# Kernel tuning notes

Hardware: AMD Instinct MI355X
Metric: run time of the kernel (lower is better)

The kernel has to match this reference:

```python
import jax, jax.numpy as jnp
import numpy as np

B, T, D = 2, 2048, 2048
N_HEADS, N_KV, HEAD_DIM = 16, 8, 128
SOFTCAP = 50.0
BIG_NEG = -2.3819763e38
ROPE_BASE = 10000.0


def apply_rope(x, positions):
    # x: [B, L, N, H], positions: [B, L]
    H = x.shape[-1]
    half = H // 2
    fraction = 2.0 * jnp.arange(half, dtype=jnp.float32) / H
    timescale = ROPE_BASE ** fraction  # [H/2]
    sinusoid = positions.astype(jnp.float32)[:, :, None, None] / timescale[None, None, None, :]  # [B,L,1,H/2]
    sin, cos = jnp.sin(sinusoid), jnp.cos(sinusoid)
    first, second = jnp.split(x, 2, axis=-1)
    out = jnp.concatenate([first * cos - second * sin, second * cos + first * sin], axis=-1)
    return out.astype(x.dtype)


def setup_inputs() -> dict:
    key = jax.random.key(0)
    k1, k2, k3, k4 = jax.random.split(key, 4)
    x = jax.random.normal(k1, (B, T, D), dtype=jnp.float32)
    positions = jnp.broadcast_to(jnp.arange(T, dtype=jnp.int32), (B, T))
    # causal mask [B, 1, T, S]
    attn_mask = jnp.broadcast_to(jnp.tril(jnp.ones((T, T), dtype=bool))[None, None], (B, 1, T, T))
    s = 1.0 / np.sqrt(D)
    w_q = jax.random.normal(k2, (N_HEADS, D, HEAD_DIM), dtype=jnp.float32) * s
    w_kv = jax.random.normal(k3, (2, N_KV, D, HEAD_DIM), dtype=jnp.float32) * s
    w_out = jax.random.normal(k4, (N_HEADS, HEAD_DIM, D), dtype=jnp.float32) * (1.0 / np.sqrt(N_HEADS * HEAD_DIM))
    return {"x": x, "positions": positions, "attn_mask": attn_mask, "w_q": w_q, "w_kv": w_kv, "w_out": w_out}


def reference(x, positions, attn_mask, w_q, w_kv, w_out):
    # projections (GQA branch: num_kv_heads != num_heads)
    q = jnp.einsum('btd,ndh->btnh', x, w_q)            # [B,T,N,H]
    kv = jnp.einsum('bsd,cndh->cbsnh', x, w_kv)        # [2,B,S,K,H]
    k, v = kv[0], kv[1]
    q = apply_rope(q, positions) * (HEAD_DIM ** -0.5)  # rsqrt_head_dim
    k = apply_rope(k, positions)
    G = N_HEADS // N_KV
    q = q.reshape(B, T, N_KV, G, HEAD_DIM)             # B T K G H
    logits = jnp.einsum('btkgh,bskh->bkgts', q, k).astype(jnp.float32)
    logits = jnp.tanh(logits / SOFTCAP) * SOFTCAP
    masked = jnp.where(attn_mask[:, :, None, :, :], logits, BIG_NEG)
    probs = jax.nn.softmax(masked, axis=-1).astype(k.dtype)
    encoded = jnp.einsum('bkgts,bskh->btkgh', probs, v).reshape(B, T, N_HEADS, HEAD_DIM)
    return jnp.einsum('btnh,nhd->btd', encoded, w_out)
```

## Files before the change

### kernel.cpp

```cpp
#include <hip/hip_runtime.h>


typedef unsigned short u16;
typedef __attribute__((ext_vector_type(8))) short short8;
typedef __attribute__((ext_vector_type(4))) float floatx4;

static __device__ __forceinline__ u16 f2b(float f){
  unsigned u = __float_as_uint(f);
  u = (u + 0x7fffu + ((u >> 16) & 1u)) >> 16;
  return (u16)u;
}
static __device__ __forceinline__ float b2f(u16 u){
  return __uint_as_float(((unsigned)u) << 16);
}
static __device__ __forceinline__ void gload16(const u16* g, u16* l){
  __builtin_amdgcn_global_load_lds(
      (const __attribute__((address_space(1))) unsigned int*)g,
      (__attribute__((address_space(3))) unsigned int*)l, 16, 0, 0);
}

static __device__ void tr64(const float* __restrict__ s, u16* __restrict__ d,
                            int sRS, int dRS, float (*t)[65], int tid){
  #pragma unroll
  for(int i = 0; i < 16; i++){
    int idx = tid + 256 * i;
    t[idx >> 6][idx & 63] = s[(long)(idx >> 6) * sRS + (idx & 63)];
  }
  __syncthreads();
  #pragma unroll
  for(int i = 0; i < 16; i++){
    int idx = tid + 256 * i;
    d[(long)(idx >> 6) * dRS + (idx & 63)] = f2b(t[idx & 63][idx >> 6]);
  }
}

__global__ __launch_bounds__(256) void k_prep(
    const float* __restrict__ x, u16* __restrict__ xb,
    const float* __restrict__ wq, u16* __restrict__ wq_t,
    const float* __restrict__ wkv, u16* __restrict__ wkv_t,
    const float* __restrict__ wo, u16* __restrict__ wo_t,
    const int* __restrict__ pos, float* __restrict__ tab){
  __shared__ float t[64][65];
  int blk = blockIdx.x, tid = threadIdx.x;
  if(blk < 8192){
    int i = blk * 256 + tid;
    float4 v = ((const float4*)x)[i];
    ushort4 o = make_ushort4(f2b(v.x), f2b(v.y), f2b(v.z), f2b(v.w));
    ((ushort4*)xb)[i] = o;
  } else if(blk < 9216){
    int q = blk - 8192;
    int bx = q & 1, by = (q >> 1) & 31, bz = q >> 6;
    tr64(wq + (long)bz * 262144 + (long)by * 64 * 128 + bx * 64,
         wq_t + (long)bz * 262144 + (long)bx * 64 * 2048 + by * 64, 128, 2048, t, tid);
  } else if(blk < 10240){
    int q = blk - 9216;
    int bx = q & 1, by = (q >> 1) & 31, bz = q >> 6;
    tr64(wkv + (long)bz * 262144 + (long)by * 64 * 128 + bx * 64,
         wkv_t + (long)bz * 262144 + (long)bx * 64 * 2048 + by * 64, 128, 2048, t, tid);
  } else if(blk < 11264){
    int q = blk - 10240;
    int bx = q & 31, by = q >> 5;
    tr64(wo + (long)by * 64 * 2048 + bx * 64,
         wo_t + (long)bx * 64 * 2048 + by * 64, 2048, 2048, t, tid);
  } else {
    int idx = (blk - 11264) * 256 + tid;
    int row = idx >> 6, h = idx & 63;
    float pf = (float)pos[row];
    float inv = exp2f(-0.20762050593045077f * (float)h);
    float ang = pf * inv;
    tab[(row << 7) + h]      = sinf(ang);
    tab[(row << 7) + 64 + h] = cosf(ang);
  }
}

__global__ __launch_bounds__(256) void k_gemm_qkv(
    const u16* __restrict__ A, const u16* __restrict__ wq_t, const u16* __restrict__ wkv_t,
    const float* __restrict__ tab,
    u16* __restrict__ qb, u16* __restrict__ kb, u16* __restrict__ vtp){
  __shared__ __attribute__((aligned(16))) u16 pool[128 * 132];
  u16* sA = pool;
  u16* sB = pool + 8192;
  int mt = blockIdx.x, nt = blockIdx.y;
  const u16* Bt = (nt < 16) ? (wq_t + (long)nt * 262144)
                            : (wkv_t + (long)(nt - 16) * 262144);
  int tid = threadIdx.x;
  int lane = tid & 63, wave = tid >> 6, l15 = lane & 15, quad = lane >> 4;
  int ro = (wave & 1) * 64, co = (wave >> 1) * 64;
  int xm7 = l15 & 7;
  int srow = tid >> 3;
  int gch  = (tid & 7) ^ (srow & 7);
  const u16* Ag = A  + ((long)(mt * 128) + srow) * 2048 + (gch << 3);
  const u16* Bg = Bt + (long)srow * 2048 + (gch << 3);
  u16* lA = sA + tid * 8;
  u16* lB = sB + tid * 8;
  floatx4 acc[4][4];
  const floatx4 fz = {0.f, 0.f, 0.f, 0.f};
  #pragma unroll
  for(int r = 0; r < 4; r++)
    #pragma unroll
    for(int c = 0; c < 4; c++) acc[r][c] = fz;
  for(int k0 = 0; k0 < 2048; k0 += 64){
    #pragma unroll
    for(int r = 0; r < 4; r++){
      gload16(Ag + (long)r * 65536 + k0, lA + r * 2048);
      gload16(Bg + (long)r * 65536 + k0, lB + r * 2048);
    }
    __syncthreads();
    #pragma unroll
    for(int ks = 0; ks < 2; ks++){
      short8 af[4], bfr[4];
      #pragma unroll
      for(int r = 0; r < 4; r++)
        af[r]  = *(const short8*)(sA + ((ro + r * 16 + l15) << 6) + ((((ks << 2) | quad) ^ xm7) << 3));
      #pragma unroll
      for(int c = 0; c < 4; c++)
        bfr[c] = *(const short8*)(sB + ((co + c * 16 + l15) << 6) + ((((ks << 2) | quad) ^ xm7) << 3));
      #pragma unroll
      for(int r = 0; r < 4; r++)
        #pragma unroll
        for(int c = 0; c < 4; c++)
          acc[r][c] = __builtin_amdgcn_mfma_f32_16x16x32_bf16(af[r], bfr[c], acc[r][c], 0, 0, 0);
    }
    __syncthreads();
  }
  u16* sT = pool;
  #pragma unroll
  for(int r = 0; r < 4; r++)
    #pragma unroll
    for(int c = 0; c < 4; c++){
      int row = ro + r * 16 + quad * 4, col = co + c * 16 + l15;
      #pragma unroll
      for(int j = 0; j < 4; j++) sT[(row + j) * 132 + col] = f2b(acc[r][c][j]);
    }
  __syncthreads();
  int grow0 = mt * 128;
  if(nt < 24){
    float scale = (nt < 16) ? 0.08838834764831845f : 1.0f;
    u16* dst = (nt < 16) ? qb : kb;
    int dS   = (nt < 16) ? 2048 : 1024;
    int dcol = (nt < 16) ? nt * 128 : (nt - 16) * 128;
    #pragma unroll
    for(int it = 0; it < 16; it++){
      int idx = tid + 256 * it;
      int row = idx >> 5, cw = idx & 31;
      int grow = grow0 + row;
      unsigned lo = *(const unsigned*)&sT[row * 132 + 2 * cw];
      unsigned hi = *(const unsigned*)&sT[row * 132 + 64 + 2 * cw];
      float2 sn = *(const float2*)&tab[(grow << 7) + 2 * cw];
      float2 cs = *(const float2*)&tab[(grow << 7) + 64 + 2 * cw];
      float x1a = b2f((u16)lo), x1b = b2f((u16)(lo >> 16));
      float x2a = b2f((u16)hi), x2b = b2f((u16)(hi >> 16));
      float o1a = (x1a * cs.x - x2a * sn.x) * scale;
      float o1b = (x1b * cs.y - x2b * sn.y) * scale;
      float o2a = (x2a * cs.x + x1a * sn.x) * scale;
      float o2b = (x2b * cs.y + x1b * sn.y) * scale;
      unsigned w1 = (unsigned)f2b(o1a) | ((unsigned)f2b(o1b) << 16);
      unsigned w2 = (unsigned)f2b(o2a) | ((unsigned)f2b(o2b) << 16);
      *(unsigned*)&dst[(long)grow * dS + dcol + 2 * cw] = w1;
      *(unsigned*)&dst[(long)grow * dS + dcol + 64 + 2 * cw] = w2;
    }
  } else {
    int b = mt >> 4, kvh = nt - 24;
    u16* vt = vtp + (long)(b * 8 + kvh) * 262144;
    int tcol0 = (mt & 15) * 128;
    int h = tid >> 1, s0 = (tid & 1) * 64;
    #pragma unroll
    for(int i = 0; i < 16; i++){
      int s = s0 + i * 4;
      ushort4 v4 = make_ushort4(sT[(s    ) * 132 + h], sT[(s + 1) * 132 + h],
                                sT[(s + 2) * 132 + h], sT[(s + 3) * 132 + h]);
      *(ushort4*)&vt[(long)h * 2048 + tcol0 + s] = v4;
    }
  }
}

__global__ __launch_bounds__(256) void k_gemm_out(
    const u16* __restrict__ A, const u16* __restrict__ Bt0, float* __restrict__ C){
  __shared__ __attribute__((aligned(16))) u16 sA[128 * 64];
  __shared__ __attribute__((aligned(16))) u16 sB[128 * 64];
  int mt = blockIdx.x, nt = blockIdx.y;
  const u16* Bt = Bt0 + (long)nt * 262144;
  int tid = threadIdx.x;
  int lane = tid & 63, wave = tid >> 6, l15 = lane & 15, quad = lane >> 4;
  int ro = (wave & 1) * 64, co = (wave >> 1) * 64;
  int xm7 = l15 & 7;
  int srow = tid >> 3;
  int gch  = (tid & 7) ^ (srow & 7);
  const u16* Ag = A  + ((long)(mt * 128) + srow) * 2048 + (gch << 3);
  const u16* Bg = Bt + (long)srow * 2048 + (gch << 3);
  u16* lA = sA + tid * 8;
  u16* lB = sB + tid * 8;
  floatx4 acc[4][4];
  const floatx4 fz = {0.f, 0.f, 0.f, 0.f};
  #pragma unroll
  for(int r = 0; r < 4; r++)
    #pragma unroll
    for(int c = 0; c < 4; c++) acc[r][c] = fz;
  for(int k0 = 0; k0 < 2048; k0 += 64){
    #pragma unroll
    for(int r = 0; r < 4; r++){
      gload16(Ag + (long)r * 65536 + k0, lA + r * 2048);
      gload16(Bg + (long)r * 65536 + k0, lB + r * 2048);
    }
    __syncthreads();
    #pragma unroll
    for(int ks = 0; ks < 2; ks++){
      short8 af[4], bfr[4];
      #pragma unroll
      for(int r = 0; r < 4; r++)
        af[r]  = *(const short8*)(sA + ((ro + r * 16 + l15) << 6) + ((((ks << 2) | quad) ^ xm7) << 3));
      #pragma unroll
      for(int c = 0; c < 4; c++)
        bfr[c] = *(const short8*)(sB + ((co + c * 16 + l15) << 6) + ((((ks << 2) | quad) ^ xm7) << 3));
      #pragma unroll
      for(int r = 0; r < 4; r++)
        #pragma unroll
        for(int c = 0; c < 4; c++)
          acc[r][c] = __builtin_amdgcn_mfma_f32_16x16x32_bf16(af[r], bfr[c], acc[r][c], 0, 0, 0);
    }
    __syncthreads();
  }
  long rb0 = (long)mt * 128 + ro + quad * 4;
  #pragma unroll
  for(int r = 0; r < 4; r++)
    #pragma unroll
    for(int c = 0; c < 4; c++){
      int col = nt * 128 + co + c * 16 + l15;
      #pragma unroll
      for(int j = 0; j < 4; j++)
        C[(rb0 + r * 16 + j) * 2048 + col] = acc[r][c][j];
    }
}

__global__ __launch_bounds__(256) void k_flash(
    const u16* __restrict__ qb, const u16* __restrict__ kb,
    const u16* __restrict__ vt, u16* __restrict__ enc){
  __shared__ __attribute__((aligned(16))) u16 sK[2 * 64 * 128];
  __shared__ __attribute__((aligned(16))) u16 sVt[2 * 128 * 64];
  __shared__ __attribute__((aligned(16))) u16 sP[4][16][72];
  int qt = 31 - blockIdx.y;
  int hidx = blockIdx.x;
  int b = hidx >> 4, kv = (hidx >> 1) & 7, g = hidx & 1;
  int tid = threadIdx.x;
  int lane = tid & 63, wave = tid >> 6, l15 = lane & 15, quad = lane >> 4;

  short8 qf[4];
  {
    const u16* qg = qb + ((long)b * 2048 + qt * 64 + wave * 16 + l15) * 2048
                       + (kv * 2 + g) * 128 + quad * 8;
    #pragma unroll
    for(int ks = 0; ks < 4; ks++) qf[ks] = *(const short8*)(qg + ks * 32);
  }

  int krow = tid >> 4;
  int kch  = (tid & 15) ^ krow;
  const u16* Kg = kb + ((long)b * 2048 + krow) * 1024 + kv * 128 + (kch << 3);
  int vrow = tid >> 3;
  int vch  = (tid & 7) ^ (vrow & 7);
  const u16* Vg = vt + ((long)(b * 8 + kv) * 128 + vrow) * 2048 + (vch << 3);
  u16* lK = sK  + tid * 8;
  u16* lV = sVt + tid * 8;
  #pragma unroll
  for(int r = 0; r < 4; r++){
    gload16(Kg + (long)r * 16384, lK + r * 2048);
    gload16(Vg + (long)r * 65536, lV + r * 2048);
  }

  float l_loc[4] = {0.f, 0.f, 0.f, 0.f};
  floatx4 o_acc[8];
  const floatx4 fz = {0.f, 0.f, 0.f, 0.f};
  #pragma unroll
  for(int c = 0; c < 8; c++) o_acc[c] = fz;

  const float c1 = 0.057707801635558536f;
  const float c2 = -144.26950408889634f;
  const float c3 = 72.13475204444817f;

  for(int kt = 0; kt <= qt; kt++){
    int buf = (kt & 1) * 8192;
    __syncthreads();
    if(kt < qt){
      int nb = buf ^ 8192;
      #pragma unroll
      for(int r = 0; r < 4; r++){
        gload16(Kg + (long)(kt + 1) * 65536 + (long)r * 16384, lK + nb + r * 2048);
        gload16(Vg + (kt + 1) * 64 + (long)r * 65536, lV + nb + r * 2048);
      }
    }
    floatx4 s_acc[4];
    #pragma unroll
    for(int c = 0; c < 4; c++) s_acc[c] = fz;
    #pragma unroll
    for(int ks = 0; ks < 4; ks++){
      #pragma unroll
      for(int cb = 0; cb < 4; cb++){
        short8 bk = *(const short8*)(sK + buf + ((cb * 16 + l15) << 7)
                                     + ((((ks << 2) | quad) ^ l15) << 3));
        s_acc[cb] = __builtin_amdgcn_mfma_f32_16x16x32_bf16(qf[ks], bk, s_acc[cb], 0, 0, 0);
      }
    }
    if(kt < qt){
      #pragma unroll
      for(int r = 0; r < 4; r++){
        #pragma unroll
        for(int cb = 0; cb < 4; cb++){
          float s = s_acc[cb][r];
          float u = __builtin_amdgcn_exp2f(c1 * s);
          float d = __builtin_amdgcn_rcpf(u + 1.f);
          float p = __builtin_amdgcn_exp2f(__builtin_fmaf(c2, d, c3));
          l_loc[r] += p;
          sP[wave][quad * 4 + r][cb * 16 + l15] = f2b(p);
        }
      }
    } else {
      int rloc = wave * 16 + quad * 4;
      #pragma unroll
      for(int r = 0; r < 4; r++){
        #pragma unroll
        for(int cb = 0; cb < 4; cb++){
          float s = s_acc[cb][r];
          float u = __builtin_amdgcn_exp2f(c1 * s);
          float d = __builtin_amdgcn_rcpf(u + 1.f);
          float p = __builtin_amdgcn_exp2f(__builtin_fmaf(c2, d, c3));
          if(cb * 16 + l15 > rloc + r) p = 0.f;
          l_loc[r] += p;
          sP[wave][quad * 4 + r][cb * 16 + l15] = f2b(p);
        }
      }
    }
    #pragma unroll
    for(int ks2 = 0; ks2 < 2; ks2++){
      short8 ap = *(const short8*)&sP[wave][l15][ks2 * 32 + quad * 8];
      #pragma unroll
      for(int c = 0; c < 8; c++){
        short8 bv = *(const short8*)(sVt + buf + ((c * 16 + l15) << 6)
                                     + ((((ks2 << 2) | quad) ^ (l15 & 7)) << 3));
        o_acc[c] = __builtin_amdgcn_mfma_f32_16x16x32_bf16(ap, bv, o_acc[c], 0, 0, 0);
      }
    }
  }
  #pragma unroll
  for(int r = 0; r < 4; r++){
    float l = l_loc[r];
    #pragma unroll
    for(int off = 1; off < 16; off <<= 1) l += __shfl_xor(l, off);
    float invl = 1.f / l;
    long rowe = (long)b * 2048 + qt * 64 + wave * 16 + quad * 4 + r;
    #pragma unroll
    for(int c = 0; c < 8; c++)
      enc[rowe * 2048 + (kv * 2 + g) * 128 + c * 16 + l15] = f2b(o_acc[c][r] * invl);
  }
}

extern "C" void kernel_launch(void* const* d_in, const int* in_sizes, int n_in,
                              void* d_out, int out_size, void* d_ws, size_t ws_size,
                              hipStream_t stream){
  const float* x     = (const float*)d_in[0];
  const int*   posi  = (const int*)  d_in[1];
  const float* w_q   = (const float*)d_in[3];
  const float* w_kv  = (const float*)d_in[4];
  const float* w_out = (const float*)d_in[5];
  float* out = (float*)d_out;

  char* w = (char*)d_ws;
  u16* xb     = (u16*)(w);
  u16* wq_t   = (u16*)(w + 16777216);
  u16* wkv_t  = (u16*)(w + 25165824);
  u16* wout_t = (u16*)(w + 33554432);
  u16* q_buf  = (u16*)(w + 41943040);
  u16* k_buf  = (u16*)(w + 58720256);
  u16* v_t    = (u16*)(w + 67108864);
  float* tab  = (float*)(w + 75497472);
  u16* enc    = xb;

  k_prep    <<<12288, 256, 0, stream>>>(x, xb, w_q, wq_t, w_kv, wkv_t, w_out, wout_t, posi, tab);
  k_gemm_qkv<<<dim3(32, 32), 256, 0, stream>>>(xb, wq_t, wkv_t, tab, q_buf, k_buf, v_t);
  k_flash   <<<dim3(32, 32), 256, 0, stream>>>(q_buf, k_buf, v_t, enc);
  k_gemm_out<<<dim3(32, 16), 256, 0, stream>>>(enc, wout_t, out);
}
```

Baseline: 333.0 us.

## Split flash-attention waves 2x2 over query rows and key columns with reduction

Each wave in the attention kernel now owns 32 query rows and half of each 64-key tile, instead of 16 rows and the full tile. Each K fragment loaded from shared memory therefore feeds two MFMAs, which cuts LDS reads per MFMA for QK^T. The two key-halves accumulate partial outputs and row sums that are combined through shared memory at the end. The P buffer is reshaped with an XOR swizzle to reduce bank conflicts. In exchange the kernel holds twice the accumulator registers, which may lower occupancy, and adds a final cross-wave reduction with extra syncs.

```diff
diff --git a/kernel.cpp b/kernel.cpp
--- a/kernel.cpp
+++ b/kernel.cpp
@@ -237,19 +237,23 @@
     const u16* __restrict__ vt, u16* __restrict__ enc){
   __shared__ __attribute__((aligned(16))) u16 sK[2 * 64 * 128];
   __shared__ __attribute__((aligned(16))) u16 sVt[2 * 128 * 64];
-  __shared__ __attribute__((aligned(16))) u16 sP[4][16][72];
+  __shared__ __attribute__((aligned(16))) u16 sP[4][32][40];
   int qt = 31 - blockIdx.y;
   int hidx = blockIdx.x;
   int b = hidx >> 4, kv = (hidx >> 1) & 7, g = hidx & 1;
   int tid = threadIdx.x;
   int lane = tid & 63, wave = tid >> 6, l15 = lane & 15, quad = lane >> 4;
-
-  short8 qf[4];
+  int rq = wave >> 1, kq = wave & 1;
+
+  short8 qf[2][4];
   {
-    const u16* qg = qb + ((long)b * 2048 + qt * 64 + wave * 16 + l15) * 2048
+    const u16* qg = qb + ((long)b * 2048 + qt * 64 + rq * 32 + l15) * 2048
                        + (kv * 2 + g) * 128 + quad * 8;
     #pragma unroll
-    for(int ks = 0; ks < 4; ks++) qf[ks] = *(const short8*)(qg + ks * 32);
+    for(int rf = 0; rf < 2; rf++)
+      #pragma unroll
+      for(int ks = 0; ks < 4; ks++)
+        qf[rf][ks] = *(const short8*)(qg + rf * 16 * 2048 + ks * 32);
   }
 
   int krow = tid >> 4;
@@ -266,11 +270,13 @@
     gload16(Vg + (long)r * 65536, lV + r * 2048);
   }
 
-  float l_loc[4] = {0.f, 0.f, 0.f, 0.f};
-  floatx4 o_acc[8];
+  float l_loc[2][4] = {{0.f,0.f,0.f,0.f},{0.f,0.f,0.f,0.f}};
+  floatx4 o_acc[2][8];
   const floatx4 fz = {0.f, 0.f, 0.f, 0.f};
   #pragma unroll
-  for(int c = 0; c < 8; c++) o_acc[c] = fz;
+  for(int rf = 0; rf < 2; rf++)
+    #pragma unroll
+    for(int c = 0; c < 8; c++) o_acc[rf][c] = fz;
 
   const float c1 = 0.057707801635558536f;
   const float c2 = -144.26950408889634f;
@@ -287,68 +293,89 @@
         gload16(Vg + (kt + 1) * 64 + (long)r * 65536, lV + nb + r * 2048);
       }
     }
-    floatx4 s_acc[4];
-    #pragma unroll
-    for(int c = 0; c < 4; c++) s_acc[c] = fz;
+    floatx4 s_acc[2][2];
+    #pragma unroll
+    for(int rf = 0; rf < 2; rf++)
+      #pragma unroll
+      for(int cf = 0; cf < 2; cf++) s_acc[rf][cf] = fz;
     #pragma unroll
     for(int ks = 0; ks < 4; ks++){
       #pragma unroll
-      for(int cb = 0; cb < 4; cb++){
-        short8 bk = *(const short8*)(sK + buf + ((cb * 16 + l15) << 7)
+      for(int cf = 0; cf < 2; cf++){
+        int row = kq * 32 + cf * 16 + l15;
+        short8 bk = *(const short8*)(sK + buf + (row << 7)
                                      + ((((ks << 2) | quad) ^ l15) << 3));
-        s_acc[cb] = __builtin_amdgcn_mfma_f32_16x16x32_bf16(qf[ks], bk, s_acc[cb], 0, 0, 0);
+        #pragma unroll
+        for(int rf = 0; rf < 2; rf++)
+          s_acc[rf][cf] = __builtin_amdgcn_mfma_f32_16x16x32_bf16(qf[rf][ks], bk, s_acc[rf][cf], 0, 0, 0);
       }
     }
-    if(kt < qt){
-      #pragma unroll
-      for(int r = 0; r < 4; r++){
-        #pragma unroll
-        for(int cb = 0; cb < 4; cb++){
-          float s = s_acc[cb][r];
+    bool diag = (kt == qt);
+    #pragma unroll
+    for(int rf = 0; rf < 2; rf++)
+      #pragma unroll
+      for(int cf = 0; cf < 2; cf++)
+        #pragma unroll
+        for(int r = 0; r < 4; r++){
+          float s = s_acc[rf][cf][r];
           float u = __builtin_amdgcn_exp2f(c1 * s);
           float d = __builtin_amdgcn_rcpf(u + 1.f);
           float p = __builtin_amdgcn_exp2f(__builtin_fmaf(c2, d, c3));
-          l_loc[r] += p;
-          sP[wave][quad * 4 + r][cb * 16 + l15] = f2b(p);
+          if(diag && (kq * 32 + cf * 16 + l15 > rq * 32 + rf * 16 + quad * 4 + r)) p = 0.f;
+          l_loc[rf][r] += p;
+          int chunk = ((cf << 1) | (l15 >> 3)) ^ r;
+          sP[wave][rf * 16 + quad * 4 + r][(chunk << 3) + (l15 & 7)] = f2b(p);
         }
+    #pragma unroll
+    for(int rf = 0; rf < 2; rf++){
+      short8 ap = *(const short8*)&sP[wave][rf * 16 + l15][(quad ^ (l15 & 3)) << 3];
+      #pragma unroll
+      for(int cf = 0; cf < 8; cf++){
+        int vrw = cf * 16 + l15;
+        short8 bv = *(const short8*)(sVt + buf + (vrw << 6)
+                                     + ((((kq << 2) | quad) ^ (l15 & 7)) << 3));
+        o_acc[rf][cf] = __builtin_amdgcn_mfma_f32_16x16x32_bf16(ap, bv, o_acc[rf][cf], 0, 0, 0);
       }
-    } else {
-      int rloc = wave * 16 + quad * 4;
+    }
+  }
+  __syncthreads();
+  float* ex  = (float*)sK;
+  float* exl = (float*)sVt;
+  if(kq == 0){
+    #pragma unroll
+    for(int rf = 0; rf < 2; rf++)
+      #pragma unroll
+      for(int cf = 0; cf < 8; cf++)
+        *(floatx4*)&ex[rq * 4096 + (rf * 8 + cf) * 256 + lane * 4] = o_acc[rf][cf];
+    #pragma unroll
+    for(int rf = 0; rf < 2; rf++)
+      #pragma unroll
+      for(int r = 0; r < 4; r++)
+        exl[rq * 512 + (rf * 4 + r) * 64 + lane] = l_loc[rf][r];
+  }
+  __syncthreads();
+  if(kq == 1){
+    #pragma unroll
+    for(int rf = 0; rf < 2; rf++)
+      #pragma unroll
+      for(int cf = 0; cf < 8; cf++){
+        floatx4 o0 = *(const floatx4*)&ex[rq * 4096 + (rf * 8 + cf) * 256 + lane * 4];
+        o_acc[rf][cf] += o0;
+      }
+    #pragma unroll
+    for(int rf = 0; rf < 2; rf++){
       #pragma unroll
       for(int r = 0; r < 4; r++){
-        #pragma unroll
-        for(int cb = 0; cb < 4; cb++){
-          float s = s_acc[cb][r];
-          float u = __builtin_amdgcn_exp2f(c1 * s);
-          float d = __builtin_amdgcn_rcpf(u + 1.f);
-          float p = __builtin_amdgcn_exp2f(__builtin_fmaf(c2, d, c3));
-          if(cb * 16 + l15 > rloc + r) p = 0.f;
-          l_loc[r] += p;
-          sP[wave][quad * 4 + r][cb * 16 + l15] = f2b(p);
-        }
+        float l = l_loc[rf][r] + exl[rq * 512 + (rf * 4 + r) * 64 + lane];
+        #pragma unroll
+        for(int off = 1; off < 16; off <<= 1) l += __shfl_xor(l, off);
+        float invl = 1.f / l;
+        long rowe = (long)b * 2048 + qt * 64 + rq * 32 + rf * 16 + quad * 4 + r;
+        #pragma unroll
+        for(int cf = 0; cf < 8; cf++)
+          enc[rowe * 2048 + (kv * 2 + g) * 128 + cf * 16 + l15] = f2b(o_acc[rf][cf][r] * invl);
       }
     }
-    #pragma unroll
-    for(int ks2 = 0; ks2 < 2; ks2++){
-      short8 ap = *(const short8*)&sP[wave][l15][ks2 * 32 + quad * 8];
-      #pragma unroll
-      for(int c = 0; c < 8; c++){
-        short8 bv = *(const short8*)(sVt + buf + ((c * 16 + l15) << 6)
-                                     + ((((ks2 << 2) | quad) ^ (l15 & 7)) << 3));
-        o_acc[c] = __builtin_amdgcn_mfma_f32_16x16x32_bf16(ap, bv, o_acc[c], 0, 0, 0);
-      }
-    }
-  }
-  #pragma unroll
-  for(int r = 0; r < 4; r++){
-    float l = l_loc[r];
-    #pragma unroll
-    for(int off = 1; off < 16; off <<= 1) l += __shfl_xor(l, off);
-    float invl = 1.f / l;
-    long rowe = (long)b * 2048 + qt * 64 + wave * 16 + quad * 4 + r;
-    #pragma unroll
-    for(int c = 0; c < 8; c++)
-      enc[rowe * 2048 + (kv * 2 + g) * 128 + c * 16 + l15] = f2b(o_acc[c][r] * invl);
   }
 }
 
```

Result: slower. 344.6 us (+3.5%).

## Process 128 query rows per flash block to reuse K/V tiles

Applied to the files above, without the earlier changes.

The flash attention kernel now has each block handle 128 query rows instead of 64. Each wave owns 32 rows, split into two 16-row fragments that share each K and V tile read from LDS. This halves the K/V global loads and LDS staging per query row, and the grid drops to 16 query tiles. The causal diagonal spans two key tiles, so the lower-half waves skip the last tile and mask at their own diagonal tile. The query tiles are also reordered to interleave heavy and light blocks. The cost is double the accumulator registers and fewer blocks, which may hurt occupancy and load balance.

```diff
diff --git a/kernel.cpp b/kernel.cpp
--- a/kernel.cpp
+++ b/kernel.cpp
@@ -238,18 +238,22 @@
   __shared__ __attribute__((aligned(16))) u16 sK[2 * 64 * 128];
   __shared__ __attribute__((aligned(16))) u16 sVt[2 * 128 * 64];
   __shared__ __attribute__((aligned(16))) u16 sP[4][16][72];
-  int qt = 31 - blockIdx.y;
+  int y = blockIdx.y;
+  int qt = (y < 8) ? (15 - y) : (y - 8);
   int hidx = blockIdx.x;
   int b = hidx >> 4, kv = (hidx >> 1) & 7, g = hidx & 1;
   int tid = threadIdx.x;
   int lane = tid & 63, wave = tid >> 6, l15 = lane & 15, quad = lane >> 4;
 
-  short8 qf[4];
+  short8 qf[2][4];
   {
-    const u16* qg = qb + ((long)b * 2048 + qt * 64 + wave * 16 + l15) * 2048
+    const u16* qg = qb + ((long)b * 2048 + qt * 128 + wave * 32 + l15) * 2048
                        + (kv * 2 + g) * 128 + quad * 8;
     #pragma unroll
-    for(int ks = 0; ks < 4; ks++) qf[ks] = *(const short8*)(qg + ks * 32);
+    for(int rf = 0; rf < 2; rf++)
+      #pragma unroll
+      for(int ks = 0; ks < 4; ks++)
+        qf[rf][ks] = *(const short8*)(qg + rf * 16 * 2048 + ks * 32);
   }
 
   int krow = tid >> 4;
@@ -266,20 +270,24 @@
     gload16(Vg + (long)r * 65536, lV + r * 2048);
   }
 
-  float l_loc[4] = {0.f, 0.f, 0.f, 0.f};
-  floatx4 o_acc[8];
+  float l_loc[2][4] = {{0.f,0.f,0.f,0.f},{0.f,0.f,0.f,0.f}};
+  floatx4 o_acc[2][8];
   const floatx4 fz = {0.f, 0.f, 0.f, 0.f};
   #pragma unroll
-  for(int c = 0; c < 8; c++) o_acc[c] = fz;
+  for(int rf = 0; rf < 2; rf++)
+    #pragma unroll
+    for(int c = 0; c < 8; c++) o_acc[rf][c] = fz;
 
   const float c1 = 0.057707801635558536f;
   const float c2 = -144.26950408889634f;
   const float c3 = 72.13475204444817f;
 
-  for(int kt = 0; kt <= qt; kt++){
+  int ktmax = 2 * qt + 1;
+  int partial_kt = 2 * qt + (wave >> 1);
+  for(int kt = 0; kt <= ktmax; kt++){
     int buf = (kt & 1) * 8192;
     __syncthreads();
-    if(kt < qt){
+    if(kt < ktmax){
       int nb = buf ^ 8192;
       #pragma unroll
       for(int r = 0; r < 4; r++){
@@ -287,69 +295,79 @@
         gload16(Vg + (kt + 1) * 64 + (long)r * 65536, lV + nb + r * 2048);
       }
     }
-    floatx4 s_acc[4];
-    #pragma unroll
-    for(int c = 0; c < 4; c++) s_acc[c] = fz;
+    if(wave < 2 && kt == ktmax) continue;
+    floatx4 s_acc[2][4];
+    #pragma unroll
+    for(int rf = 0; rf < 2; rf++)
+      #pragma unroll
+      for(int cb = 0; cb < 4; cb++) s_acc[rf][cb] = fz;
     #pragma unroll
     for(int ks = 0; ks < 4; ks++){
       #pragma unroll
       for(int cb = 0; cb < 4; cb++){
         short8 bk = *(const short8*)(sK + buf + ((cb * 16 + l15) << 7)
                                      + ((((ks << 2) | quad) ^ l15) << 3));
-        s_acc[cb] = __builtin_amdgcn_mfma_f32_16x16x32_bf16(qf[ks], bk, s_acc[cb], 0, 0, 0);
+        #pragma unroll
+        for(int rf = 0; rf < 2; rf++)
+          s_acc[rf][cb] = __builtin_amdgcn_mfma_f32_16x16x32_bf16(qf[rf][ks], bk, s_acc[rf][cb], 0, 0, 0);
       }
     }
-    if(kt < qt){
-      #pragma unroll
-      for(int r = 0; r < 4; r++){
-        #pragma unroll
-        for(int cb = 0; cb < 4; cb++){
-          float s = s_acc[cb][r];
-          float u = __builtin_amdgcn_exp2f(c1 * s);
-          float d = __builtin_amdgcn_rcpf(u + 1.f);
-          float p = __builtin_amdgcn_exp2f(__builtin_fmaf(c2, d, c3));
-          l_loc[r] += p;
-          sP[wave][quad * 4 + r][cb * 16 + l15] = f2b(p);
+    bool pm = (kt == partial_kt);
+    #pragma unroll
+    for(int rf = 0; rf < 2; rf++){
+      int lr0 = wave * 32 + rf * 16 + quad * 4;
+      int lk0 = (wave >> 1) * 64;
+      if(pm){
+        #pragma unroll
+        for(int r = 0; r < 4; r++)
+          #pragma unroll
+          for(int cb = 0; cb < 4; cb++){
+            float s = s_acc[rf][cb][r];
+            float u = __builtin_amdgcn_exp2f(c1 * s);
+            float d = __builtin_amdgcn_rcpf(u + 1.f);
+            float p = __builtin_amdgcn_exp2f(__builtin_fmaf(c2, d, c3));
+            if(lk0 + cb * 16 + l15 > lr0 + r) p = 0.f;
+            l_loc[rf][r] += p;
+            sP[wave][quad * 4 + r][cb * 16 + l15] = f2b(p);
+          }
+      } else {
+        #pragma unroll
+        for(int r = 0; r < 4; r++)
+          #pragma unroll
+          for(int cb = 0; cb < 4; cb++){
+            float s = s_acc[rf][cb][r];
+            float u = __builtin_amdgcn_exp2f(c1 * s);
+            float d = __builtin_amdgcn_rcpf(u + 1.f);
+            float p = __builtin_amdgcn_exp2f(__builtin_fmaf(c2, d, c3));
+            l_loc[rf][r] += p;
+            sP[wave][quad * 4 + r][cb * 16 + l15] = f2b(p);
+          }
+      }
+      #pragma unroll
+      for(int ks2 = 0; ks2 < 2; ks2++){
+        short8 ap = *(const short8*)&sP[wave][l15][ks2 * 32 + quad * 8];
+        #pragma unroll
+        for(int cf = 0; cf < 8; cf++){
+          short8 bv = *(const short8*)(sVt + buf + ((cf * 16 + l15) << 6)
+                                       + ((((ks2 << 2) | quad) ^ (l15 & 7)) << 3));
+          o_acc[rf][cf] = __builtin_amdgcn_mfma_f32_16x16x32_bf16(ap, bv, o_acc[rf][cf], 0, 0, 0);
         }
       }
-    } else {
-      int rloc = wave * 16 + quad * 4;
-      #pragma unroll
-      for(int r = 0; r < 4; r++){
-        #pragma unroll
-        for(int cb = 0; cb < 4; cb++){
-          float s = s_acc[cb][r];
-          float u = __builtin_amdgcn_exp2f(c1 * s);
-          float d = __builtin_amdgcn_rcpf(u + 1.f);
-          float p = __builtin_amdgcn_exp2f(__builtin_fmaf(c2, d, c3));
-          if(cb * 16 + l15 > rloc + r) p = 0.f;
-          l_loc[r] += p;
-          sP[wave][quad * 4 + r][cb * 16 + l15] = f2b(p);
-        }
-      }
-    }
-    #pragma unroll
-    for(int ks2 = 0; ks2 < 2; ks2++){
-      short8 ap = *(const short8*)&sP[wave][l15][ks2 * 32 + quad * 8];
-      #pragma unroll
-      for(int c = 0; c < 8; c++){
-        short8 bv = *(const short8*)(sVt + buf + ((c * 16 + l15) << 6)
-                                     + ((((ks2 << 2) | quad) ^ (l15 & 7)) << 3));
-        o_acc[c] = __builtin_amdgcn_mfma_f32_16x16x32_bf16(ap, bv, o_acc[c], 0, 0, 0);
-      }
-    }
-  }
-  #pragma unroll
-  for(int r = 0; r < 4; r++){
-    float l = l_loc[r];
-    #pragma unroll
-    for(int off = 1; off < 16; off <<= 1) l += __shfl_xor(l, off);
-    float invl = 1.f / l;
-    long rowe = (long)b * 2048 + qt * 64 + wave * 16 + quad * 4 + r;
-    #pragma unroll
-    for(int c = 0; c < 8; c++)
-      enc[rowe * 2048 + (kv * 2 + g) * 128 + c * 16 + l15] = f2b(o_acc[c][r] * invl);
-  }
+    }
+  }
+  #pragma unroll
+  for(int rf = 0; rf < 2; rf++)
+    #pragma unroll
+    for(int r = 0; r < 4; r++){
+      float l = l_loc[rf][r];
+      #pragma unroll
+      for(int off = 1; off < 16; off <<= 1) l += __shfl_xor(l, off);
+      float invl = 1.f / l;
+      long rowe = (long)b * 2048 + qt * 128 + wave * 32 + rf * 16 + quad * 4 + r;
+      #pragma unroll
+      for(int cf = 0; cf < 8; cf++)
+        enc[rowe * 2048 + (kv * 2 + g) * 128 + cf * 16 + l15] = f2b(o_acc[rf][cf][r] * invl);
+    }
 }
 
 extern "C" void kernel_launch(void* const* d_in, const int* in_sizes, int n_in,
@@ -375,6 +393,6 @@
 
   k_prep    <<<12288, 256, 0, stream>>>(x, xb, w_q, wq_t, w_kv, wkv_t, w_out, wout_t, posi, tab);
   k_gemm_qkv<<<dim3(32, 32), 256, 0, stream>>>(xb, wq_t, wkv_t, tab, q_buf, k_buf, v_t);
-  k_flash   <<<dim3(32, 32), 256, 0, stream>>>(q_buf, k_buf, v_t, enc);
+  k_flash   <<<dim3(32, 16), 256, 0, stream>>>(q_buf, k_buf, v_t, enc);
   k_gemm_out<<<dim3(32, 16), 256, 0, stream>>>(enc, wout_t, out);
 }
```

Measured after the change: 354.0 us. 6.3% more time.
